# Optimization experiments

Measured on AMD Instinct MI355X. Metric: run time of the kernel, lower is better.

Reference implementation:

```python
import jax, jax.numpy as jnp
import numpy as np

D_MODEL = 768
H = 12
D_K = D_MODEL // H


def setup_inputs() -> dict:
    key = jax.random.key(0)
    ks = jax.random.split(key, 12)
    B, S = 2, 2048
    scale = 1.0 / np.sqrt(D_MODEL)
    q = jax.random.normal(ks[0], (B, S, D_MODEL), jnp.float32)
    k = jax.random.normal(ks[1], (B, S, D_MODEL), jnp.float32)
    v = jax.random.normal(ks[2], (B, S, D_MODEL), jnp.float32)
    mask = jnp.tril(jnp.ones((S, S), jnp.int32))[None, None]  # causal [1,1,S,S]
    wq = jax.random.normal(ks[3], (D_MODEL, D_MODEL), jnp.float32) * scale
    wk = jax.random.normal(ks[4], (D_MODEL, D_MODEL), jnp.float32) * scale
    wv = jax.random.normal(ks[5], (D_MODEL, D_MODEL), jnp.float32) * scale
    wo = jax.random.normal(ks[6], (D_MODEL, D_MODEL), jnp.float32) * scale
    bq = jax.random.normal(ks[7], (D_MODEL,), jnp.float32) * 0.02
    bk = jax.random.normal(ks[8], (D_MODEL,), jnp.float32) * 0.02
    bv = jax.random.normal(ks[9], (D_MODEL,), jnp.float32) * 0.02
    bo = jax.random.normal(ks[10], (D_MODEL,), jnp.float32) * 0.02
    return {"q": q, "k": k, "v": v, "mask": mask,
            "wq": wq, "bq": bq, "wk": wk, "bk": bk,
            "wv": wv, "bv": bv, "wo": wo, "bo": bo}


def reference(q, k, v, mask, wq, bq, wk, bk, wv, bv, wo, bo):
    B, S, _ = q.shape
    # projections (torch Linear: x @ W.T + b)
    qh = (q @ wq.T + bq).reshape(B, S, H, D_K).transpose(0, 2, 1, 3)  # [B,H,S,Dk]
    kh = (k @ wk.T + bk).reshape(B, S, H, D_K).transpose(0, 2, 1, 3)
    vh = (v @ wv.T + bv).reshape(B, S, H, D_K).transpose(0, 2, 1, 3)
    scores = jnp.einsum('bhqd,bhkd->bhqk', qh, kh) / np.sqrt(D_K)
    scores = jnp.where(mask == 0, -jnp.inf, scores)
    attn = jax.nn.softmax(scores, axis=-1)  # dropout p=0.0 (eval) -> identity
    x = jnp.einsum('bhqk,bhkd->bhqd', attn, vh)
    x = x.transpose(0, 2, 1, 3).reshape(B, S, D_MODEL)
    return x @ wo.T + bo
```

## Files before the change

kernel.cpp:

```cpp
#include <hip/hip_runtime.h>
#include <hip/hip_bf16.h>

#define DM 768
#define NH 12
#define DK 64
#define SEQ 2048
#define NB 2
#define M_ (NB*SEQ)
#define XN 3145728
#define WN 589824

typedef __bf16 bf16;
typedef bf16 bf16x2 __attribute__((ext_vector_type(2)));
typedef bf16 bf16x4 __attribute__((ext_vector_type(4)));
typedef bf16 bf16x8 __attribute__((ext_vector_type(8)));
typedef float f32x4 __attribute__((ext_vector_type(4)));

__device__ __forceinline__ f32x4 mfma16(bf16x8 a, bf16x8 b, f32x4 c) {
    return __builtin_amdgcn_mfma_f32_16x16x32_bf16(a, b, c, 0, 0, 0);
}

__device__ __forceinline__ void gload_lds16(const bf16* g, bf16* l) {
    __builtin_amdgcn_global_load_lds(
        (const __attribute__((address_space(1))) void*)g,
        (__attribute__((address_space(3))) void*)l, 16, 0, 0);
}

__global__ __launch_bounds__(256) void convert_kernel(
    const float* __restrict__ q, const float* __restrict__ k, const float* __restrict__ v,
    const float* __restrict__ wq, const float* __restrict__ wk, const float* __restrict__ wv,
    const float* __restrict__ wo, bf16* __restrict__ Xb, bf16* __restrict__ Wb)
{
    long long e = ((long long)blockIdx.x * 256 + threadIdx.x) * 8;
    const float* src; bf16* dst;
    if (e < 3LL * XN) {
        int z = (int)(e / XN);
        src = (z == 0 ? q : z == 1 ? k : v) + (e - (long long)z * XN);
        dst = Xb + e;
    } else {
        long long e2 = e - 3LL * XN;
        int z = (int)(e2 / WN);
        src = (z == 0 ? wq : z == 1 ? wk : z == 2 ? wv : wo) + (e2 - (long long)z * WN);
        dst = Wb + e2;
    }
    f32x4 a = *(const f32x4*)src;
    f32x4 b = *(const f32x4*)(src + 4);
    bf16x8 o;
#pragma unroll
    for (int j = 0; j < 4; ++j) { o[j] = (bf16)a[j]; o[j + 4] = (bf16)b[j]; }
    *(bf16x8*)dst = o;
}

__global__ __launch_bounds__(256) void qkv_gemm_kernel(
    const bf16* __restrict__ Xb, const bf16* __restrict__ Wb,
    const float* __restrict__ bq, const float* __restrict__ bk, const float* __restrict__ bv,
    bf16* __restrict__ Qh, bf16* __restrict__ Kh, bf16* __restrict__ Vt)
{
    __shared__ bf16 lds[12288];
    int z = blockIdx.z;
    const bf16* Ab = Xb + (size_t)z * XN;
    const bf16* Wz = Wb + (size_t)z * WN;
    const float* Bi = (z == 0) ? bq : (z == 1) ? bk : bv;

    int t = threadIdx.x;
    int lane = t & 63, w = t >> 6;
    int g = lane >> 4, c = lane & 15;
    int wm = (w >> 1) * 64, wn = (w & 1) * 32;
    int m0 = blockIdx.x * 128, n0 = blockIdx.y * 64;

    f32x4 acc[4][2] = {};

    const bf16* Agp[4];
#pragma unroll
    for (int r = 0; r < 4; ++r) {
        int e = r * 2048 + t * 8;
        int kk = e >> 12, mm = (e & 4095) >> 5, k8 = e & 31;
        Agp[r] = Ab + (size_t)(m0 + mm) * DM + kk * 32 + k8;
    }
    const bf16* Bgp[2];
#pragma unroll
    for (int r = 0; r < 2; ++r) {
        int e = r * 2048 + t * 8;
        int kk = e >> 11, nn = (e & 2047) >> 5, k8 = e & 31;
        Bgp[r] = Wz + (size_t)(n0 + nn) * DM + kk * 32 + k8;
    }

    for (int kt = 0; kt < 12; ++kt) {
#pragma unroll
        for (int r = 0; r < 4; ++r)
            gload_lds16(Agp[r] + kt * 64, &lds[r * 2048 + t * 8]);
#pragma unroll
        for (int r = 0; r < 2; ++r)
            gload_lds16(Bgp[r] + kt * 64, &lds[8192 + r * 2048 + t * 8]);
        __syncthreads();
        bf16x8 af[4][2], bfr[2][2];
#pragma unroll
        for (int kk = 0; kk < 2; ++kk) {
#pragma unroll
            for (int mi = 0; mi < 4; ++mi)
                af[mi][kk] = *(const bf16x8*)&lds[kk * 4096 + (wm + mi * 16 + c) * 32 + g * 8];
#pragma unroll
            for (int ni = 0; ni < 2; ++ni)
                bfr[ni][kk] = *(const bf16x8*)&lds[8192 + kk * 2048 + (wn + ni * 16 + c) * 32 + g * 8];
        }
#pragma unroll
        for (int mi = 0; mi < 4; ++mi)
#pragma unroll
            for (int ni = 0; ni < 2; ++ni) {
                acc[mi][ni] = mfma16(af[mi][0], bfr[ni][0], acc[mi][ni]);
                acc[mi][ni] = mfma16(af[mi][1], bfr[ni][1], acc[mi][ni]);
            }
        __syncthreads();
    }

    int b_ = m0 >> 11, sbase = m0 & (SEQ - 1);
    int h = blockIdx.y;
    if (z == 0) {
#pragma unroll
        for (int ni = 0; ni < 2; ++ni) {
            int nl = wn + ni * 16 + c;
            float bias = Bi[n0 + nl];
#pragma unroll
            for (int mi = 0; mi < 4; ++mi)
#pragma unroll
                for (int r = 0; r < 4; ++r) {
                    int s = sbase + wm + mi * 16 + g * 4 + r;
                    Qh[((size_t)(b_ * NH + h) * SEQ + s) * DK + nl] = (bf16)(acc[mi][ni][r] + bias);
                }
        }
    } else if (z == 1) {
#pragma unroll
        for (int ni = 0; ni < 2; ++ni) {
            int nl = wn + ni * 16 + c;
            float bias = Bi[n0 + nl];
            int chunk = nl >> 3, e = nl & 7;
#pragma unroll
            for (int mi = 0; mi < 4; ++mi)
#pragma unroll
                for (int r = 0; r < 4; ++r) {
                    int s = sbase + wm + mi * 16 + g * 4 + r;
                    int pos = ((chunk ^ (s & 7)) << 3) + e;
                    Kh[((size_t)(b_ * NH + h) * SEQ + s) * DK + pos] = (bf16)(acc[mi][ni][r] + bias);
                }
        }
    } else {
#pragma unroll
        for (int ni = 0; ni < 2; ++ni) {
            int nl = wn + ni * 16 + c;
            float bias = Bi[n0 + nl];
#pragma unroll
            for (int mi = 0; mi < 4; ++mi) {
                bf16x4 pk;
#pragma unroll
                for (int r = 0; r < 4; ++r) pk[r] = (bf16)(acc[mi][ni][r] + bias);
                int sb = wm + mi * 16;
                int grp64 = sb >> 6, grp = (sb >> 5) & 1, bb = (sb >> 4) & 1;
                int chi = 4 * grp + g;
                int col = grp64 * 64 + ((chi ^ (nl & 7)) << 3) + 4 * bb;
                *(bf16x4*)&lds[nl * 136 + col] = pk;
            }
        }
        __syncthreads();
        int dk = t >> 2, sc = (t & 3) * 32;
        bf16* vdst = Vt + ((size_t)(b_ * NH + h) * DK + dk) * SEQ + sbase + sc;
#pragma unroll
        for (int j = 0; j < 4; ++j)
            *(bf16x8*)(vdst + j * 8) = *(const bf16x8*)&lds[dk * 136 + sc + j * 8];
    }
}

__global__ __launch_bounds__(256) void o_gemm_kernel(
    const bf16* __restrict__ Xo, const bf16* __restrict__ Wo,
    const float* __restrict__ bo, float* __restrict__ out)
{
    __shared__ bf16 lds[12288];
    int t = threadIdx.x;
    int lane = t & 63, w = t >> 6;
    int g = lane >> 4, c = lane & 15;
    int wm = (w >> 1) * 64, wn = (w & 1) * 32;
    int m0 = blockIdx.x * 128, n0 = blockIdx.y * 64;

    f32x4 acc[4][2] = {};

    const bf16* Agp[4];
#pragma unroll
    for (int r = 0; r < 4; ++r) {
        int e = r * 2048 + t * 8;
        int kk = e >> 12, mm = (e & 4095) >> 5, k8 = e & 31;
        Agp[r] = Xo + (size_t)(m0 + mm) * DM + kk * 32 + k8;
    }
    const bf16* Bgp[2];
#pragma unroll
    for (int r = 0; r < 2; ++r) {
        int e = r * 2048 + t * 8;
        int kk = e >> 11, nn = (e & 2047) >> 5, k8 = e & 31;
        Bgp[r] = Wo + (size_t)(n0 + nn) * DM + kk * 32 + k8;
    }

    for (int kt = 0; kt < 12; ++kt) {
#pragma unroll
        for (int r = 0; r < 4; ++r)
            gload_lds16(Agp[r] + kt * 64, &lds[r * 2048 + t * 8]);
#pragma unroll
        for (int r = 0; r < 2; ++r)
            gload_lds16(Bgp[r] + kt * 64, &lds[8192 + r * 2048 + t * 8]);
        __syncthreads();
        bf16x8 af[4][2], bfr[2][2];
#pragma unroll
        for (int kk = 0; kk < 2; ++kk) {
#pragma unroll
            for (int mi = 0; mi < 4; ++mi)
                af[mi][kk] = *(const bf16x8*)&lds[kk * 4096 + (wm + mi * 16 + c) * 32 + g * 8];
#pragma unroll
            for (int ni = 0; ni < 2; ++ni)
                bfr[ni][kk] = *(const bf16x8*)&lds[8192 + kk * 2048 + (wn + ni * 16 + c) * 32 + g * 8];
        }
#pragma unroll
        for (int mi = 0; mi < 4; ++mi)
#pragma unroll
            for (int ni = 0; ni < 2; ++ni) {
                acc[mi][ni] = mfma16(af[mi][0], bfr[ni][0], acc[mi][ni]);
                acc[mi][ni] = mfma16(af[mi][1], bfr[ni][1], acc[mi][ni]);
            }
        __syncthreads();
    }

#pragma unroll
    for (int ni = 0; ni < 2; ++ni) {
        int n = n0 + wn + ni * 16 + c;
        float bias = bo[n];
#pragma unroll
        for (int mi = 0; mi < 4; ++mi)
#pragma unroll
            for (int r = 0; r < 4; ++r)
                out[(size_t)(m0 + wm + mi * 16 + g * 4 + r) * DM + n] = acc[mi][ni][r] + bias;
    }
}

__global__ __launch_bounds__(128) void attn_kernel(
    const bf16* __restrict__ Qh, const bf16* __restrict__ Kh, const bf16* __restrict__ Vt,
    bf16* __restrict__ Xo)
{
    __shared__ bf16 kt_lds[2][4096];
    __shared__ bf16 vt_lds[2][4096];

    int blk = blockIdx.x;
    int bh = blk % (NB * NH);
    int J  = 63 - blk / (NB * NH);
    int t = threadIdx.x;
    int w = t >> 6, lane = t & 63;
    int g = lane >> 4, c = lane & 15;
    int sw = c & 7;
    const bf16* Qb = Qh + (size_t)bh * SEQ * DK;
    const bf16* Kb = Kh + (size_t)bh * SEQ * DK;
    const bf16* Vb = Vt + (size_t)bh * DK * SEQ;
    int b_ = bh / NH, h = bh % NH;

    const float SCL = 0.125f * 1.4426950408889634f;

    int qa = J * 32 + w * 16;
    bf16x8 qf0 = *(const bf16x8*)(Qb + (size_t)(qa + c) * DK + g * 8);
    bf16x8 qf1 = *(const bf16x8*)(Qb + (size_t)(qa + c) * DK + 32 + g * 8);

    float m_st = -INFINITY, l_st = 0.f;
    f32x4 o[4] = {};
    int myq = qa + c;
    int nkt = (J >> 1) + 1;

    auto stage = [&](int kt, int buf) {
        int kb = kt * 64;
        const bf16* kg = Kb + (size_t)kb * DK + t * 8;
#pragma unroll
        for (int i = 0; i < 4; ++i)
            gload_lds16(kg + i * 1024, &kt_lds[buf][i * 1024 + t * 8]);
        int dvr = t >> 3, colc = (t & 7) * 8;
        const bf16* vg = Vb + (size_t)dvr * SEQ + kb + colc;
#pragma unroll
        for (int i = 0; i < 4; ++i)
            gload_lds16(vg + (size_t)(16 * i) * SEQ, &vt_lds[buf][i * 1024 + t * 8]);
    };

    stage(0, 0);
    for (int kt = 0; kt < nkt; ++kt) {
        __syncthreads();
        if (kt + 1 < nkt) stage(kt + 1, (kt + 1) & 1);
        int kb = kt * 64;
        int buf = kt & 1;
        bf16x8 kf[4][2];
#pragma unroll
        for (int i = 0; i < 4; ++i) {
            kf[i][0] = *(const bf16x8*)&kt_lds[buf][(16 * i + c) * 64 + ((g ^ sw) << 3)];
            kf[i][1] = *(const bf16x8*)&kt_lds[buf][(16 * i + c) * 64 + (((4 + g) ^ sw) << 3)];
        }
        bf16x8 vf[2][4];
#pragma unroll
        for (int grp = 0; grp < 2; ++grp)
#pragma unroll
            for (int t2 = 0; t2 < 4; ++t2)
                vf[grp][t2] = *(const bf16x8*)&vt_lds[buf][(16 * t2 + c) * 64 + (((grp * 4 + g) ^ sw) << 3)];

        bool masked = (kb + 63 > qa);
        float p_[4][4];
#pragma unroll
        for (int i = 0; i < 4; ++i) {
            f32x4 a = {};
            a = mfma16(kf[i][0], qf0, a);
            a = mfma16(kf[i][1], qf1, a);
            if (masked) {
#pragma unroll
                for (int r = 0; r < 4; ++r) {
                    int key = kb + i * 16 + g * 4 + r;
                    p_[i][r] = (key <= myq) ? a[r] * SCL : -INFINITY;
                }
            } else {
#pragma unroll
                for (int r = 0; r < 4; ++r) p_[i][r] = a[r] * SCL;
            }
        }
        float m0_ = fmaxf(fmaxf(p_[0][0], p_[0][1]), fmaxf(p_[0][2], p_[0][3]));
        float m1_ = fmaxf(fmaxf(p_[1][0], p_[1][1]), fmaxf(p_[1][2], p_[1][3]));
        float m2_ = fmaxf(fmaxf(p_[2][0], p_[2][1]), fmaxf(p_[2][2], p_[2][3]));
        float m3_ = fmaxf(fmaxf(p_[3][0], p_[3][1]), fmaxf(p_[3][2], p_[3][3]));
        float mx = fmaxf(fmaxf(m0_, m1_), fmaxf(m2_, m3_));
        mx = fmaxf(mx, __shfl_xor(mx, 16, 64));
        mx = fmaxf(mx, __shfl_xor(mx, 32, 64));
        float m_new = fmaxf(m_st, mx);
        float alpha = exp2f(m_st - m_new);
        m_st = m_new;
#pragma unroll
        for (int i = 0; i < 4; ++i)
#pragma unroll
            for (int r = 0; r < 4; ++r)
                p_[i][r] = exp2f(p_[i][r] - m_new);
        float s0_ = (p_[0][0] + p_[0][1]) + (p_[0][2] + p_[0][3]);
        float s1_ = (p_[1][0] + p_[1][1]) + (p_[1][2] + p_[1][3]);
        float s2_ = (p_[2][0] + p_[2][1]) + (p_[2][2] + p_[2][3]);
        float s3_ = (p_[3][0] + p_[3][1]) + (p_[3][2] + p_[3][3]);
        float psum = (s0_ + s1_) + (s2_ + s3_);
        psum += __shfl_xor(psum, 16, 64);
        psum += __shfl_xor(psum, 32, 64);
        l_st = l_st * alpha + psum;
#pragma unroll
        for (int t2 = 0; t2 < 4; ++t2)
#pragma unroll
            for (int r = 0; r < 4; ++r) o[t2][r] *= alpha;
        bf16x8 pa0, pa1;
#pragma unroll
        for (int jj = 0; jj < 8; ++jj) {
            pa0[jj] = (bf16)p_[jj >> 2][jj & 3];
            pa1[jj] = (bf16)p_[2 + (jj >> 2)][jj & 3];
        }
#pragma unroll
        for (int t2 = 0; t2 < 4; ++t2) {
            o[t2] = mfma16(vf[0][t2], pa0, o[t2]);
            o[t2] = mfma16(vf[1][t2], pa1, o[t2]);
        }
    }

    float inv = 1.f / l_st;
#pragma unroll
    for (int t2 = 0; t2 < 4; ++t2) {
        bf16x4 sa;
#pragma unroll
        for (int r = 0; r < 4; ++r) sa[r] = (bf16)(o[t2][r] * inv);
        *(bf16x4*)&Xo[(size_t)(b_ * SEQ + qa + c) * DM + h * DK + t2 * 16 + g * 4] = sa;
    }
}

extern "C" void kernel_launch(void* const* d_in, const int* in_sizes, int n_in,
                              void* d_out, int out_size, void* d_ws, size_t ws_size,
                              hipStream_t stream) {
    const float* q  = (const float*)d_in[0];
    const float* k  = (const float*)d_in[1];
    const float* v  = (const float*)d_in[2];
    const float* wq = (const float*)d_in[4];
    const float* bq = (const float*)d_in[5];
    const float* wk = (const float*)d_in[6];
    const float* bk = (const float*)d_in[7];
    const float* wv = (const float*)d_in[8];
    const float* bv = (const float*)d_in[9];
    const float* wo = (const float*)d_in[10];
    const float* bo = (const float*)d_in[11];

    bf16* Xb = (bf16*)d_ws;
    bf16* Wb = Xb + 3 * (size_t)XN;
    bf16* Qh = Wb + 4 * (size_t)WN;
    bf16* Kh = Qh + (size_t)XN;
    bf16* Vt = Kh + (size_t)XN;
    bf16* Xo = Xb;
    float* out = (float*)d_out;

    dim3 blk(256);
    convert_kernel<<<dim3(5760), blk, 0, stream>>>(q, k, v, wq, wk, wv, wo, Xb, Wb);
    qkv_gemm_kernel<<<dim3(M_ / 128, DM / 64, 3), blk, 0, stream>>>(
        Xb, Wb, bq, bk, bv, Qh, Kh, Vt);
    attn_kernel<<<dim3(24 * 64), dim3(128), 0, stream>>>(Qh, Kh, Vt, Xo);
    o_gemm_kernel<<<dim3(M_ / 128, DM / 64), blk, 0, stream>>>(Xo, Wb + 3 * (size_t)WN, bo, out);
}
```

Before: 205.0 us.

## Split causal attention KV range in two and merge partial softmax results

```diff
diff --git a/kernel.cpp b/kernel.cpp
--- a/kernel.cpp
+++ b/kernel.cpp
@@ -237,16 +237,18 @@
     }
 }
 
-__global__ __launch_bounds__(128) void attn_kernel(
+__global__ __launch_bounds__(128) void attn_part_kernel(
     const bf16* __restrict__ Qh, const bf16* __restrict__ Kh, const bf16* __restrict__ Vt,
-    bf16* __restrict__ Xo)
+    bf16* __restrict__ Po, float* __restrict__ Pml)
 {
     __shared__ bf16 kt_lds[2][4096];
     __shared__ bf16 vt_lds[2][4096];
 
     int blk = blockIdx.x;
     int bh = blk % (NB * NH);
-    int J  = 63 - blk / (NB * NH);
+    int idx = blk / (NB * NH);
+    int J = 63 - (idx >> 1);
+    int s = idx & 1;
     int t = threadIdx.x;
     int w = t >> 6, lane = t & 63;
     int g = lane >> 4, c = lane & 15;
@@ -254,117 +256,156 @@
     const bf16* Qb = Qh + (size_t)bh * SEQ * DK;
     const bf16* Kb = Kh + (size_t)bh * SEQ * DK;
     const bf16* Vb = Vt + (size_t)bh * DK * SEQ;
-    int b_ = bh / NH, h = bh % NH;
 
     const float SCL = 0.125f * 1.4426950408889634f;
 
     int qa = J * 32 + w * 16;
-    bf16x8 qf0 = *(const bf16x8*)(Qb + (size_t)(qa + c) * DK + g * 8);
-    bf16x8 qf1 = *(const bf16x8*)(Qb + (size_t)(qa + c) * DK + 32 + g * 8);
+    int myq = qa + c;
+    int nkt = (J >> 1) + 1;
+    int tiles0 = (nkt + 1) >> 1;
+    int kt_begin = s ? tiles0 : 0;
+    int kt_end   = s ? nkt : tiles0;
 
     float m_st = -INFINITY, l_st = 0.f;
     f32x4 o[4] = {};
-    int myq = qa + c;
-    int nkt = (J >> 1) + 1;
-
-    auto stage = [&](int kt, int buf) {
-        int kb = kt * 64;
-        const bf16* kg = Kb + (size_t)kb * DK + t * 8;
-#pragma unroll
-        for (int i = 0; i < 4; ++i)
-            gload_lds16(kg + i * 1024, &kt_lds[buf][i * 1024 + t * 8]);
-        int dvr = t >> 3, colc = (t & 7) * 8;
-        const bf16* vg = Vb + (size_t)dvr * SEQ + kb + colc;
-#pragma unroll
-        for (int i = 0; i < 4; ++i)
-            gload_lds16(vg + (size_t)(16 * i) * SEQ, &vt_lds[buf][i * 1024 + t * 8]);
-    };
-
-    stage(0, 0);
-    for (int kt = 0; kt < nkt; ++kt) {
-        __syncthreads();
-        if (kt + 1 < nkt) stage(kt + 1, (kt + 1) & 1);
-        int kb = kt * 64;
-        int buf = kt & 1;
-        bf16x8 kf[4][2];
-#pragma unroll
-        for (int i = 0; i < 4; ++i) {
-            kf[i][0] = *(const bf16x8*)&kt_lds[buf][(16 * i + c) * 64 + ((g ^ sw) << 3)];
-            kf[i][1] = *(const bf16x8*)&kt_lds[buf][(16 * i + c) * 64 + (((4 + g) ^ sw) << 3)];
-        }
-        bf16x8 vf[2][4];
-#pragma unroll
-        for (int grp = 0; grp < 2; ++grp)
+
+    if (kt_begin < kt_end) {
+        bf16x8 qf0 = *(const bf16x8*)(Qb + (size_t)(qa + c) * DK + g * 8);
+        bf16x8 qf1 = *(const bf16x8*)(Qb + (size_t)(qa + c) * DK + 32 + g * 8);
+
+        auto stage = [&](int kt, int buf) {
+            int kb = kt * 64;
+            const bf16* kg = Kb + (size_t)kb * DK + t * 8;
+#pragma unroll
+            for (int i = 0; i < 4; ++i)
+                gload_lds16(kg + i * 1024, &kt_lds[buf][i * 1024 + t * 8]);
+            int dvr = t >> 3, colc = (t & 7) * 8;
+            const bf16* vg = Vb + (size_t)dvr * SEQ + kb + colc;
+#pragma unroll
+            for (int i = 0; i < 4; ++i)
+                gload_lds16(vg + (size_t)(16 * i) * SEQ, &vt_lds[buf][i * 1024 + t * 8]);
+        };
+
+        stage(kt_begin, kt_begin & 1);
+        for (int kt = kt_begin; kt < kt_end; ++kt) {
+            __syncthreads();
+            if (kt + 1 < kt_end) stage(kt + 1, (kt + 1) & 1);
+            int kb = kt * 64;
+            int buf = kt & 1;
+            bf16x8 kf[4][2];
+#pragma unroll
+            for (int i = 0; i < 4; ++i) {
+                kf[i][0] = *(const bf16x8*)&kt_lds[buf][(16 * i + c) * 64 + ((g ^ sw) << 3)];
+                kf[i][1] = *(const bf16x8*)&kt_lds[buf][(16 * i + c) * 64 + (((4 + g) ^ sw) << 3)];
+            }
+            bf16x8 vf[2][4];
+#pragma unroll
+            for (int grp = 0; grp < 2; ++grp)
+#pragma unroll
+                for (int t2 = 0; t2 < 4; ++t2)
+                    vf[grp][t2] = *(const bf16x8*)&vt_lds[buf][(16 * t2 + c) * 64 + (((grp * 4 + g) ^ sw) << 3)];
+
+            bool masked = (kb + 63 > qa);
+            float p_[4][4];
+#pragma unroll
+            for (int i = 0; i < 4; ++i) {
+                f32x4 a = {};
+                a = mfma16(kf[i][0], qf0, a);
+                a = mfma16(kf[i][1], qf1, a);
+                if (masked) {
+#pragma unroll
+                    for (int r = 0; r < 4; ++r) {
+                        int key = kb + i * 16 + g * 4 + r;
+                        p_[i][r] = (key <= myq) ? a[r] * SCL : -INFINITY;
+                    }
+                } else {
+#pragma unroll
+                    for (int r = 0; r < 4; ++r) p_[i][r] = a[r] * SCL;
+                }
+            }
+            float m0_ = fmaxf(fmaxf(p_[0][0], p_[0][1]), fmaxf(p_[0][2], p_[0][3]));
+            float m1_ = fmaxf(fmaxf(p_[1][0], p_[1][1]), fmaxf(p_[1][2], p_[1][3]));
+            float m2_ = fmaxf(fmaxf(p_[2][0], p_[2][1]), fmaxf(p_[2][2], p_[2][3]));
+            float m3_ = fmaxf(fmaxf(p_[3][0], p_[3][1]), fmaxf(p_[3][2], p_[3][3]));
+            float mx = fmaxf(fmaxf(m0_, m1_), fmaxf(m2_, m3_));
+            mx = fmaxf(mx, __shfl_xor(mx, 16, 64));
+            mx = fmaxf(mx, __shfl_xor(mx, 32, 64));
+            float m_new = fmaxf(m_st, mx);
+            float alpha = exp2f(m_st - m_new);
+            m_st = m_new;
+#pragma unroll
+            for (int i = 0; i < 4; ++i)
+#pragma unroll
+                for (int r = 0; r < 4; ++r)
+                    p_[i][r] = exp2f(p_[i][r] - m_new);
+            float s0_ = (p_[0][0] + p_[0][1]) + (p_[0][2] + p_[0][3]);
+            float s1_ = (p_[1][0] + p_[1][1]) + (p_[1][2] + p_[1][3]);
+            float s2_ = (p_[2][0] + p_[2][1]) + (p_[2][2] + p_[2][3]);
+            float s3_ = (p_[3][0] + p_[3][1]) + (p_[3][2] + p_[3][3]);
+            float psum = (s0_ + s1_) + (s2_ + s3_);
+            psum += __shfl_xor(psum, 16, 64);
+            psum += __shfl_xor(psum, 32, 64);
+            l_st = l_st * alpha + psum;
 #pragma unroll
             for (int t2 = 0; t2 < 4; ++t2)
-                vf[grp][t2] = *(const bf16x8*)&vt_lds[buf][(16 * t2 + c) * 64 + (((grp * 4 + g) ^ sw) << 3)];
-
-        bool masked = (kb + 63 > qa);
-        float p_[4][4];
-#pragma unroll
-        for (int i = 0; i < 4; ++i) {
-            f32x4 a = {};
-            a = mfma16(kf[i][0], qf0, a);
-            a = mfma16(kf[i][1], qf1, a);
-            if (masked) {
-#pragma unroll
-                for (int r = 0; r < 4; ++r) {
-                    int key = kb + i * 16 + g * 4 + r;
-                    p_[i][r] = (key <= myq) ? a[r] * SCL : -INFINITY;
-                }
-            } else {
-#pragma unroll
-                for (int r = 0; r < 4; ++r) p_[i][r] = a[r] * SCL;
-            }
-        }
-        float m0_ = fmaxf(fmaxf(p_[0][0], p_[0][1]), fmaxf(p_[0][2], p_[0][3]));
-        float m1_ = fmaxf(fmaxf(p_[1][0], p_[1][1]), fmaxf(p_[1][2], p_[1][3]));
-        float m2_ = fmaxf(fmaxf(p_[2][0], p_[2][1]), fmaxf(p_[2][2], p_[2][3]));
-        float m3_ = fmaxf(fmaxf(p_[3][0], p_[3][1]), fmaxf(p_[3][2], p_[3][3]));
-        float mx = fmaxf(fmaxf(m0_, m1_), fmaxf(m2_, m3_));
-        mx = fmaxf(mx, __shfl_xor(mx, 16, 64));
-        mx = fmaxf(mx, __shfl_xor(mx, 32, 64));
-        float m_new = fmaxf(m_st, mx);
-        float alpha = exp2f(m_st - m_new);
-        m_st = m_new;
-#pragma unroll
-        for (int i = 0; i < 4; ++i)
-#pragma unroll
-            for (int r = 0; r < 4; ++r)
-                p_[i][r] = exp2f(p_[i][r] - m_new);
-        float s0_ = (p_[0][0] + p_[0][1]) + (p_[0][2] + p_[0][3]);
-        float s1_ = (p_[1][0] + p_[1][1]) + (p_[1][2] + p_[1][3]);
-        float s2_ = (p_[2][0] + p_[2][1]) + (p_[2][2] + p_[2][3]);
-        float s3_ = (p_[3][0] + p_[3][1]) + (p_[3][2] + p_[3][3]);
-        float psum = (s0_ + s1_) + (s2_ + s3_);
-        psum += __shfl_xor(psum, 16, 64);
-        psum += __shfl_xor(psum, 32, 64);
-        l_st = l_st * alpha + psum;
-#pragma unroll
-        for (int t2 = 0; t2 < 4; ++t2)
-#pragma unroll
-            for (int r = 0; r < 4; ++r) o[t2][r] *= alpha;
-        bf16x8 pa0, pa1;
-#pragma unroll
-        for (int jj = 0; jj < 8; ++jj) {
-            pa0[jj] = (bf16)p_[jj >> 2][jj & 3];
-            pa1[jj] = (bf16)p_[2 + (jj >> 2)][jj & 3];
-        }
-#pragma unroll
-        for (int t2 = 0; t2 < 4; ++t2) {
-            o[t2] = mfma16(vf[0][t2], pa0, o[t2]);
-            o[t2] = mfma16(vf[1][t2], pa1, o[t2]);
-        }
-    }
-
-    float inv = 1.f / l_st;
+#pragma unroll
+                for (int r = 0; r < 4; ++r) o[t2][r] *= alpha;
+            bf16x8 pa0, pa1;
+#pragma unroll
+            for (int jj = 0; jj < 8; ++jj) {
+                pa0[jj] = (bf16)p_[jj >> 2][jj & 3];
+                pa1[jj] = (bf16)p_[2 + (jj >> 2)][jj & 3];
+            }
+#pragma unroll
+            for (int t2 = 0; t2 < 4; ++t2) {
+                o[t2] = mfma16(vf[0][t2], pa0, o[t2]);
+                o[t2] = mfma16(vf[1][t2], pa1, o[t2]);
+            }
+        }
+    }
+
+    size_t base = ((((size_t)bh * 64 + J) * 2 + s) * 32 + w * 16 + c);
+    if (g == 0) { Pml[base * 2] = m_st; Pml[base * 2 + 1] = l_st; }
 #pragma unroll
     for (int t2 = 0; t2 < 4; ++t2) {
         bf16x4 sa;
 #pragma unroll
-        for (int r = 0; r < 4; ++r) sa[r] = (bf16)(o[t2][r] * inv);
-        *(bf16x4*)&Xo[(size_t)(b_ * SEQ + qa + c) * DM + h * DK + t2 * 16 + g * 4] = sa;
-    }
+        for (int r = 0; r < 4; ++r) sa[r] = (bf16)o[t2][r];
+        *(bf16x4*)&Po[base * 64 + t2 * 16 + g * 4] = sa;
+    }
+}
+
+__global__ __launch_bounds__(256) void attn_merge_kernel(
+    const bf16* __restrict__ Po, const float* __restrict__ Pml, bf16* __restrict__ Xo)
+{
+    int idx = blockIdx.x * 256 + threadIdx.x;
+    int row = idx >> 2;
+    int dq = (idx & 3) * 16;
+    int bh = row >> 11;
+    int rem = row & 2047;
+    int J = rem >> 5, q = rem & 31;
+    size_t b0 = (((size_t)bh * 64 + J) * 2 + 0) * 32 + q;
+    size_t b1 = b0 + 32;
+    float m0 = Pml[b0 * 2], l0 = Pml[b0 * 2 + 1];
+    float m1 = Pml[b1 * 2], l1 = Pml[b1 * 2 + 1];
+    float mM = fmaxf(m0, m1);
+    float sc0 = exp2f(m0 - mM), sc1 = exp2f(m1 - mM);
+    float inv = 1.f / (sc0 * l0 + sc1 * l1);
+    sc0 *= inv; sc1 *= inv;
+    int b_ = bh / NH, h = bh % NH;
+    bf16* xrow = Xo + (size_t)(b_ * SEQ + J * 32 + q) * DM + h * DK + dq;
+    const bf16* p0 = Po + b0 * 64 + dq;
+    const bf16* p1 = Po + b1 * 64 + dq;
+    bf16x8 v0a = *(const bf16x8*)p0, v0b = *(const bf16x8*)(p0 + 8);
+    bf16x8 v1a = *(const bf16x8*)p1, v1b = *(const bf16x8*)(p1 + 8);
+    bf16x8 oa, ob2;
+#pragma unroll
+    for (int j = 0; j < 8; ++j) {
+        oa[j]  = (bf16)(sc0 * (float)v0a[j] + sc1 * (float)v1a[j]);
+        ob2[j] = (bf16)(sc0 * (float)v0b[j] + sc1 * (float)v1b[j]);
+    }
+    *(bf16x8*)xrow = oa;
+    *(bf16x8*)(xrow + 8) = ob2;
 }
 
 extern "C" void kernel_launch(void* const* d_in, const int* in_sizes, int n_in,
@@ -387,6 +428,8 @@
     bf16* Qh = Wb + 4 * (size_t)WN;
     bf16* Kh = Qh + (size_t)XN;
     bf16* Vt = Kh + (size_t)XN;
+    bf16* Po = Vt + (size_t)XN;
+    float* Pml = (float*)(Po + 6291456);
     bf16* Xo = Xb;
     float* out = (float*)d_out;
 
@@ -394,6 +437,7 @@
     convert_kernel<<<dim3(5760), blk, 0, stream>>>(q, k, v, wq, wk, wv, wo, Xb, Wb);
     qkv_gemm_kernel<<<dim3(M_ / 128, DM / 64, 3), blk, 0, stream>>>(
         Xb, Wb, bq, bk, bv, Qh, Kh, Vt);
-    attn_kernel<<<dim3(24 * 64), dim3(128), 0, stream>>>(Qh, Kh, Vt, Xo);
+    attn_part_kernel<<<dim3(24 * 64 * 2), dim3(128), 0, stream>>>(Qh, Kh, Vt, Po, Pml);
+    attn_merge_kernel<<<dim3(768), blk, 0, stream>>>(Po, Pml, Xo);
     o_gemm_kernel<<<dim3(M_ / 128, DM / 64), blk, 0, stream>>>(Xo, Wb + 3 * (size_t)WN, bo, out);
 }
```

Measured after the change: 206.7 us. About the same (+0.8%).
